# Kernel optimization log

Measured on AMD Instinct MI355X. Metric: run time of the kernel, lower is better.

Reference implementation:

```python
import jax, jax.numpy as jnp
import numpy as np

B, N, T, F = 4, 256, 16, 128
H = 256

def setup_inputs() -> dict:
    key = jax.random.key(0)
    k1, k2, k3, k4, k5 = jax.random.split(key, 5)
    bound1 = 1.0 / np.sqrt(2 * F)
    bound2 = 1.0 / np.sqrt(H)
    return {
        "nodefeat": jax.random.normal(k1, (B, N, T, F), dtype=jnp.float32),
        "W1": jax.random.uniform(k2, (H, 2 * F), minval=-bound1, maxval=bound1, dtype=jnp.float32),
        "b1": jax.random.uniform(k3, (H,), minval=-bound1, maxval=bound1, dtype=jnp.float32),
        "W2": jax.random.uniform(k4, (1, H), minval=-bound2, maxval=bound2, dtype=jnp.float32),
        "b2": jax.random.uniform(k5, (1,), minval=-bound2, maxval=bound2, dtype=jnp.float32),
    }

def reference(nodefeat, W1, b1, W2, b2):
    # nodefeat: [B,N,T,F] -> mean over time -> h: [B,N,F]
    h = jnp.mean(nodefeat, axis=2)
    f = h.shape[-1]
    # Split W1 to avoid materializing the [B,N,N,2F] concat:
    # Linear(cat(h_i,h_j)) = h_i @ W1[:, :F].T + h_j @ W1[:, F:].T + b1
    a = jnp.einsum('bnf,hf->bnh', h, W1[:, :f])  # contribution of h_i
    c = jnp.einsum('bnf,hf->bnh', h, W1[:, f:])  # contribution of h_j
    pre = a[:, :, None, :] + c[:, None, :, :] + b1  # [B,N,N,H]
    act = jax.nn.relu(pre)
    logits = jnp.einsum('bijh,h->bij', act, W2[0]) + b2[0]  # [B,N,N]
    return logits
```

## Files before the change

### kernel.cpp

```cpp
#include <hip/hip_runtime.h>

#define B_ 4
#define N_ 256
#define T_ 16
#define F_ 128
#define H_ 256

__global__ __launch_bounds__(1024) void lp_k1(const float* __restrict__ nf,
                                              const float* __restrict__ W1,
                                              const float* __restrict__ b1,
                                              float* __restrict__ aT,
                                              float* __restrict__ cT) {
    __shared__ float sh[F_ * 4];
    __shared__ float red[8 * 1024];

    const int tile = blockIdx.x;
    const int bn0  = tile * 4;
    const int b    = bn0 >> 8;
    const int n0   = bn0 & 255;
    const int tid  = threadIdx.x;

    {
        const int gh = tid >> 9;
        const int p  = tid & 511;
        const int n  = p >> 7;
        const int f  = p & 127;
        const float* src = nf + (size_t)(bn0 + n) * (T_ * F_) + gh * 8 * F_ + f;
        float s = 0.f;
#pragma unroll
        for (int t = 0; t < 8; ++t) s += src[t * F_];
        red[tid] = s;
    }
    __syncthreads();
    if (tid < 512) {
        const int n = tid >> 7;
        const int f = tid & 127;
        sh[f * 4 + n] = (red[tid] + red[512 + tid]) * (1.0f / 16.0f);
    }
    __syncthreads();

    const int kq = tid >> 8;
    const int h  = tid & 255;
    const float* w1a = W1 + (size_t)h * (2 * F_) + kq * 32;
    const float* w1c = w1a + F_;
    const float* shk = sh + kq * 32 * 4;

    float acca[4] = {0.f, 0.f, 0.f, 0.f};
    float accc[4] = {0.f, 0.f, 0.f, 0.f};

#pragma unroll
    for (int kk = 0; kk < 32; kk += 4) {
        const float4 wa = *(const float4*)(w1a + kk);
        const float4 wc = *(const float4*)(w1c + kk);
        const float wav[4] = {wa.x, wa.y, wa.z, wa.w};
        const float wcv[4] = {wc.x, wc.y, wc.z, wc.w};
#pragma unroll
        for (int e = 0; e < 4; ++e) {
            const float4 hv = *(const float4*)(shk + (kk + e) * 4);
            acca[0] = fmaf(hv.x, wav[e], acca[0]);
            acca[1] = fmaf(hv.y, wav[e], acca[1]);
            acca[2] = fmaf(hv.z, wav[e], acca[2]);
            acca[3] = fmaf(hv.w, wav[e], acca[3]);
            accc[0] = fmaf(hv.x, wcv[e], accc[0]);
            accc[1] = fmaf(hv.y, wcv[e], accc[1]);
            accc[2] = fmaf(hv.z, wcv[e], accc[2]);
            accc[3] = fmaf(hv.w, wcv[e], accc[3]);
        }
    }

#pragma unroll
    for (int e = 0; e < 4; ++e) {
        red[(e)     * 1024 + kq * 256 + h] = acca[e];
        red[(4 + e) * 1024 + kq * 256 + h] = accc[e];
    }
    __syncthreads();

    if (tid < 256) {
        float ra[4], rc[4];
#pragma unroll
        for (int e = 0; e < 4; ++e) {
            const float* pa = red + e * 1024 + tid;
            const float* pc = red + (4 + e) * 1024 + tid;
            ra[e] = (pa[0] + pa[256]) + (pa[512] + pa[768]);
            rc[e] = (pc[0] + pc[256]) + (pc[512] + pc[768]);
        }
        const float bb = b1[tid];
        *(float4*)(aT + (size_t)tile * (H_ * 4) + tid * 4) =
            make_float4(ra[0] + bb, ra[1] + bb, ra[2] + bb, ra[3] + bb);
        *(float4*)(cT + ((size_t)b * H_ + tid) * N_ + n0) =
            make_float4(rc[0], rc[1], rc[2], rc[3]);
    }
}

__global__ __launch_bounds__(1024) void lp_k2(const float* __restrict__ aT,
                                              const float* __restrict__ cT,
                                              const float* __restrict__ W2,
                                              const float* __restrict__ b2,
                                              float* __restrict__ out) {
    __shared__ float sa[H_ * 4];
    __shared__ float pr[4][4][256];

    const int tile = blockIdx.x;
    const int bn0  = tile * 4;
    const int b    = bn0 >> 8;
    const int i0   = bn0 & 255;
    const int tid  = threadIdx.x;
    const int hq   = tid >> 8;
    const int j    = tid & 255;

    sa[tid] = aT[(size_t)tile * (H_ * 4) + tid];
    __syncthreads();

    const float* crow = cT + (size_t)b * (H_ * N_) + j;
    const int h0 = hq * 64;

    float acc0 = 0.f, acc1 = 0.f, acc2 = 0.f, acc3 = 0.f;

#pragma unroll 4
    for (int hh = 0; hh < 64; ++hh) {
        const int h = h0 + hh;
        const float cj = crow[(size_t)h * N_];
        const float w  = W2[h];
        const float4 av = *(const float4*)(sa + h * 4);
        float x;
        x = av.x + cj; acc0 = fmaf(fmaxf(x, 0.f), w, acc0);
        x = av.y + cj; acc1 = fmaf(fmaxf(x, 0.f), w, acc1);
        x = av.z + cj; acc2 = fmaf(fmaxf(x, 0.f), w, acc2);
        x = av.w + cj; acc3 = fmaf(fmaxf(x, 0.f), w, acc3);
    }

    pr[0][hq][j] = acc0;
    pr[1][hq][j] = acc1;
    pr[2][hq][j] = acc2;
    pr[3][hq][j] = acc3;
    __syncthreads();

    {
        const int r  = tid >> 8;
        const int jj = tid & 255;
        const float s = (pr[r][0][jj] + pr[r][1][jj]) + (pr[r][2][jj] + pr[r][3][jj]);
        out[((size_t)b * N_ + (i0 + r)) * N_ + jj] = s + b2[0];
    }
}

extern "C" void kernel_launch(void* const* d_in, const int* in_sizes, int n_in,
                              void* d_out, int out_size, void* d_ws, size_t ws_size,
                              hipStream_t stream) {
    const float* nodefeat = (const float*)d_in[0];
    const float* W1       = (const float*)d_in[1];
    const float* b1       = (const float*)d_in[2];
    const float* W2       = (const float*)d_in[3];
    const float* b2       = (const float*)d_in[4];
    float* out = (float*)d_out;

    float* aT = (float*)d_ws;
    float* cT = aT + (size_t)256 * H_ * 4;

    lp_k1<<<256, 1024, 0, stream>>>(nodefeat, W1, b1, aT, cT);
    lp_k2<<<256, 1024, 0, stream>>>(aT, cT, W2, b2, out);
}
```

Before: 25.43 us.

## Split prep into mean/W1-transpose kernel and separate coalesced projection GEMM

Result: no change. 25.69 us (+1.0%).

```diff
diff --git a/kernel.cpp b/kernel.cpp
--- a/kernel.cpp
+++ b/kernel.cpp
@@ -5,90 +5,93 @@
 #define T_ 16
 #define F_ 128
 #define H_ 256
+#define BN_ (B_ * N_)
 
-__global__ __launch_bounds__(1024) void lp_k1(const float* __restrict__ nf,
-                                              const float* __restrict__ W1,
-                                              const float* __restrict__ b1,
-                                              float* __restrict__ aT,
-                                              float* __restrict__ cT) {
-    __shared__ float sh[F_ * 4];
-    __shared__ float red[8 * 1024];
-
-    const int tile = blockIdx.x;
-    const int bn0  = tile * 4;
-    const int b    = bn0 >> 8;
-    const int n0   = bn0 & 255;
-    const int tid  = threadIdx.x;
-
-    {
-        const int gh = tid >> 9;
-        const int p  = tid & 511;
-        const int n  = p >> 7;
-        const int f  = p & 127;
-        const float* src = nf + (size_t)(bn0 + n) * (T_ * F_) + gh * 8 * F_ + f;
+__global__ __launch_bounds__(1024) void lp_prep(const float* __restrict__ nf,
+                                                const float* __restrict__ W1,
+                                                float* __restrict__ hbar,
+                                                float* __restrict__ W1T) {
+    __shared__ float sT[64][65];
+    const int tid = threadIdx.x;
+    if (blockIdx.x < 128) {
+        const int idx = blockIdx.x * 1024 + tid;
+        const int bn  = idx >> 7;
+        const int f   = idx & 127;
+        const float* src = nf + (size_t)bn * (T_ * F_) + f;
         float s = 0.f;
 #pragma unroll
-        for (int t = 0; t < 8; ++t) s += src[t * F_];
-        red[tid] = s;
+        for (int t = 0; t < T_; ++t) s += src[t * F_];
+        hbar[idx] = s * (1.0f / 16.0f);
+    } else {
+        const int t  = blockIdx.x - 128;
+        const int y0 = (t >> 2) * 64;
+        const int x0 = (t & 3) * 64;
+        const int ty = tid >> 6;
+        const int tx = tid & 63;
+#pragma unroll
+        for (int r = 0; r < 4; ++r)
+            sT[r * 16 + ty][tx] = W1[(size_t)(y0 + r * 16 + ty) * 256 + (x0 + tx)];
+        __syncthreads();
+#pragma unroll
+        for (int r = 0; r < 4; ++r)
+            W1T[(size_t)(x0 + r * 16 + ty) * 256 + (y0 + tx)] = sT[tx][r * 16 + ty];
     }
-    __syncthreads();
-    if (tid < 512) {
-        const int n = tid >> 7;
-        const int f = tid & 127;
-        sh[f * 4 + n] = (red[tid] + red[512 + tid]) * (1.0f / 16.0f);
-    }
-    __syncthreads();
+}
 
-    const int kq = tid >> 8;
-    const int h  = tid & 255;
-    const float* w1a = W1 + (size_t)h * (2 * F_) + kq * 32;
-    const float* w1c = w1a + F_;
-    const float* shk = sh + kq * 32 * 4;
+__global__ __launch_bounds__(512) void lp_gemm(const float* __restrict__ hbar,
+                                               const float* __restrict__ W1T,
+                                               const float* __restrict__ b1,
+                                               float* __restrict__ aT,
+                                               float* __restrict__ cT) {
+    __shared__ float red[16][4][128];
 
-    float acca[4] = {0.f, 0.f, 0.f, 0.f};
-    float accc[4] = {0.f, 0.f, 0.f, 0.f};
+    const int tile8 = blockIdx.x >> 1;
+    const int h0    = (blockIdx.x & 1) * 128;
+    const int bn0   = tile8 * 8;
+    const int b     = bn0 >> 8;
+    const int tid   = threadIdx.x;
+    const int kq    = __builtin_amdgcn_readfirstlane(tid >> 7);
+    const int hl    = tid & 127;
+    const int h     = h0 + hl;
 
+    const float* wA = W1T + (size_t)(kq * 32) * H_ + h;
+    const float* wC = W1T + (size_t)(F_ + kq * 32) * H_ + h;
+    const float* hb = hbar + (size_t)bn0 * F_ + kq * 32;
+
+    float acca[8] = {0.f, 0.f, 0.f, 0.f, 0.f, 0.f, 0.f, 0.f};
+    float accc[8] = {0.f, 0.f, 0.f, 0.f, 0.f, 0.f, 0.f, 0.f};
+
+#pragma unroll 4
+    for (int kk = 0; kk < 32; ++kk) {
+        const float wa = wA[(size_t)kk * H_];
+        const float wc = wC[(size_t)kk * H_];
 #pragma unroll
-    for (int kk = 0; kk < 32; kk += 4) {
-        const float4 wa = *(const float4*)(w1a + kk);
-        const float4 wc = *(const float4*)(w1c + kk);
-        const float wav[4] = {wa.x, wa.y, wa.z, wa.w};
-        const float wcv[4] = {wc.x, wc.y, wc.z, wc.w};
-#pragma unroll
-        for (int e = 0; e < 4; ++e) {
-            const float4 hv = *(const float4*)(shk + (kk + e) * 4);
-            acca[0] = fmaf(hv.x, wav[e], acca[0]);
-            acca[1] = fmaf(hv.y, wav[e], acca[1]);
-            acca[2] = fmaf(hv.z, wav[e], acca[2]);
-            acca[3] = fmaf(hv.w, wav[e], acca[3]);
-            accc[0] = fmaf(hv.x, wcv[e], accc[0]);
-            accc[1] = fmaf(hv.y, wcv[e], accc[1]);
-            accc[2] = fmaf(hv.z, wcv[e], accc[2]);
-            accc[3] = fmaf(hv.w, wcv[e], accc[3]);
+        for (int n = 0; n < 8; ++n) {
+            const float hv = hb[n * F_ + kk];
+            acca[n] = fmaf(hv, wa, acca[n]);
+            accc[n] = fmaf(hv, wc, accc[n]);
         }
     }
 
 #pragma unroll
-    for (int e = 0; e < 4; ++e) {
-        red[(e)     * 1024 + kq * 256 + h] = acca[e];
-        red[(4 + e) * 1024 + kq * 256 + h] = accc[e];
+    for (int n = 0; n < 8; ++n) {
+        red[n][kq][hl]     = acca[n];
+        red[8 + n][kq][hl] = accc[n];
     }
     __syncthreads();
 
-    if (tid < 256) {
-        float ra[4], rc[4];
+    const int rv = tid >> 7;
 #pragma unroll
-        for (int e = 0; e < 4; ++e) {
-            const float* pa = red + e * 1024 + tid;
-            const float* pc = red + (4 + e) * 1024 + tid;
-            ra[e] = (pa[0] + pa[256]) + (pa[512] + pa[768]);
-            rc[e] = (pc[0] + pc[256]) + (pc[512] + pc[768]);
+    for (int i = 0; i < 4; ++i) {
+        const int v = rv * 4 + i;
+        const float s = (red[v][0][hl] + red[v][1][hl]) + (red[v][2][hl] + red[v][3][hl]);
+        if (v < 8) {
+            const int bn = bn0 + v;
+            aT[((size_t)(bn >> 2) * H_ + h) * 4 + (bn & 3)] = s + b1[h];
+        } else {
+            const int n = v - 8;
+            cT[((size_t)b * H_ + h) * N_ + ((bn0 & 255) + n)] = s;
         }
-        const float bb = b1[tid];
-        *(float4*)(aT + (size_t)tile * (H_ * 4) + tid * 4) =
-            make_float4(ra[0] + bb, ra[1] + bb, ra[2] + bb, ra[3] + bb);
-        *(float4*)(cT + ((size_t)b * H_ + tid) * N_ + n0) =
-            make_float4(rc[0], rc[1], rc[2], rc[3]);
     }
 }
 
@@ -97,7 +100,6 @@
                                               const float* __restrict__ W2,
                                               const float* __restrict__ b2,
                                               float* __restrict__ out) {
-    __shared__ float sa[H_ * 4];
     __shared__ float pr[4][4][256];
 
     const int tile = blockIdx.x;
@@ -105,23 +107,21 @@
     const int b    = bn0 >> 8;
     const int i0   = bn0 & 255;
     const int tid  = threadIdx.x;
-    const int hq   = tid >> 8;
+    const int hq   = __builtin_amdgcn_readfirstlane(tid >> 8);
     const int j    = tid & 255;
 
-    sa[tid] = aT[(size_t)tile * (H_ * 4) + tid];
-    __syncthreads();
-
     const float* crow = cT + (size_t)b * (H_ * N_) + j;
+    const float* arow = aT + (size_t)tile * (H_ * 4);
     const int h0 = hq * 64;
 
     float acc0 = 0.f, acc1 = 0.f, acc2 = 0.f, acc3 = 0.f;
 
-#pragma unroll 4
+#pragma unroll 8
     for (int hh = 0; hh < 64; ++hh) {
         const int h = h0 + hh;
         const float cj = crow[(size_t)h * N_];
         const float w  = W2[h];
-        const float4 av = *(const float4*)(sa + h * 4);
+        const float4 av = *(const float4*)(arow + h * 4);
         float x;
         x = av.x + cj; acc0 = fmaf(fmaxf(x, 0.f), w, acc0);
         x = av.y + cj; acc1 = fmaf(fmaxf(x, 0.f), w, acc1);
@@ -135,12 +135,10 @@
     pr[3][hq][j] = acc3;
     __syncthreads();
 
-    {
-        const int r  = tid >> 8;
-        const int jj = tid & 255;
-        const float s = (pr[r][0][jj] + pr[r][1][jj]) + (pr[r][2][jj] + pr[r][3][jj]);
-        out[((size_t)b * N_ + (i0 + r)) * N_ + jj] = s + b2[0];
-    }
+    const int r  = tid >> 8;
+    const int jj = tid & 255;
+    const float s = (pr[r][0][jj] + pr[r][1][jj]) + (pr[r][2][jj] + pr[r][3][jj]);
+    out[((size_t)b * N_ + (i0 + r)) * N_ + jj] = s + b2[0];
 }
 
 extern "C" void kernel_launch(void* const* d_in, const int* in_sizes, int n_in,
@@ -153,9 +151,12 @@
     const float* b2       = (const float*)d_in[4];
     float* out = (float*)d_out;
 
-    float* aT = (float*)d_ws;
-    float* cT = aT + (size_t)256 * H_ * 4;
+    float* hbar = (float*)d_ws;
+    float* W1T  = hbar + (size_t)BN_ * F_;
+    float* aT   = W1T + 256 * 256;
+    float* cT   = aT + (size_t)256 * H_ * 4;
 
-    lp_k1<<<256, 1024, 0, stream>>>(nodefeat, W1, b1, aT, cT);
+    lp_prep<<<144, 1024, 0, stream>>>(nodefeat, W1, hbar, W1T);
+    lp_gemm<<<256, 512, 0, stream>>>(hbar, W1T, b1, aT, cT);
     lp_k2<<<256, 1024, 0, stream>>>(aT, cT, W2, b2, out);
 }
```
